# Performance work log

Measured on AMD Instinct MI355X. Metric: run time of the kernel, lower is better.

## Reference

```python
import jax, jax.numpy as jnp
import numpy as np

DIMS = 1024
HEAD = 16
CTX = 2048
BATCH = 2


def setup_inputs() -> dict:
    key = jax.random.key(0)
    ks = jax.random.split(key, 8)
    s = 0.02
    x = jax.random.normal(ks[0], (BATCH, CTX, DIMS), dtype=jnp.float32)
    Wq = jax.random.normal(ks[1], (DIMS, DIMS), dtype=jnp.float32) * s
    bq = jax.random.normal(ks[2], (DIMS,), dtype=jnp.float32) * s
    Wk = jax.random.normal(ks[3], (DIMS, DIMS), dtype=jnp.float32) * s  # k Linear has bias=False
    Wv = jax.random.normal(ks[4], (DIMS, DIMS), dtype=jnp.float32) * s
    bv = jax.random.normal(ks[5], (DIMS,), dtype=jnp.float32) * s
    Wout = jax.random.normal(ks[6], (DIMS, DIMS), dtype=jnp.float32) * s
    bout = jax.random.normal(ks[7], (DIMS,), dtype=jnp.float32) * s
    factor = jnp.asarray(0.0005, dtype=jnp.float32)
    return {"x": x, "Wq": Wq, "bq": bq, "Wk": Wk, "Wv": Wv, "bv": bv,
            "Wout": Wout, "bout": bout, "factor": factor}


def reference(x, Wq, bq, Wk, Wv, bv, Wout, bout, factor):
    b, ctx, dims = x.shape
    head = HEAD
    hd = dims // head
    scale = hd ** (-0.25)  # note: torch uses (dims // head) ** -0.25

    q = x @ Wq.T + bq
    k = x @ Wk.T
    v = x @ Wv.T + bv

    # (b, head, ctx, hd)
    q = q.reshape(b, ctx, head, hd).transpose(0, 2, 1, 3)
    k = k.reshape(b, ctx, head, hd).transpose(0, 2, 1, 3)
    v = v.reshape(b, ctx, head, hd).transpose(0, 2, 1, 3)

    # per-key scaling: keys whose first feature is exactly 0 get clamped softplus(Factor)
    zero_factor = jnp.clip(jax.nn.softplus(factor), 0.0, 0.001)
    scaled_zero = jnp.where(k[:, :, :, 0] == 0, zero_factor, jnp.ones((), x.dtype))  # (b,h,ctx)

    qk = jnp.einsum('bhqd,bhkd->bhqk', q * scale, k * scale)
    qk = qk * scaled_zero[:, :, None, :]  # broadcast over query dim
    qk = qk.astype(jnp.float32)

    w = jax.nn.softmax(qk, axis=-1)  # temperature = 1.0
    wv = jnp.einsum('bhqk,bhkd->bqhd', w, v).reshape(b, ctx, dims)

    # faithful to source: out projection applied twice (inside _forward, then in forward)
    out1 = wv @ Wout.T + bout
    out = out1 @ Wout.T + bout
    return out, qk
```

## Files before the change

kernel.cpp:

```cpp
#include <hip/hip_runtime.h>

typedef unsigned short u16;
typedef __bf16 bf16x8 __attribute__((ext_vector_type(8)));
typedef float f32x4 __attribute__((ext_vector_type(4)));
typedef unsigned int u32x4 __attribute__((ext_vector_type(4)));

__device__ __forceinline__ u16 f2b(float f) {
    union { float f; unsigned u; } c; c.f = f;
    unsigned r = (c.u + 0x7fffu + ((c.u >> 16) & 1u)) >> 16;
    return (u16)r;
}

__device__ __forceinline__ bf16x8 ldlds(const u16* p) {
    return __builtin_bit_cast(bf16x8, *(const u32x4*)p);
}

__device__ __forceinline__ void stage8(const float* s, u16* d) {
    float4 a = *(const float4*)s;
    float4 b = *(const float4*)(s + 4);
    ushort4 lo; lo.x = f2b(a.x); lo.y = f2b(a.y); lo.z = f2b(a.z); lo.w = f2b(a.w);
    ushort4 hi; hi.x = f2b(b.x); hi.y = f2b(b.y); hi.z = f2b(b.z); hi.w = f2b(b.w);
    *(ushort4*)d = lo;
    *(ushort4*)(d + 4) = hi;
}
__device__ __forceinline__ void stage8(const u16* s, u16* d) {
    *(u32x4*)d = *(const u32x4*)s;
}

__device__ __forceinline__ void cstore(float v, u16* p) { *p = f2b(v); }
__device__ __forceinline__ void cstore(float v, float* p) { *p = v; }

__global__ __launch_bounds__(256) void cvt_bf16(
    const float* __restrict__ in, u16* __restrict__ out, int n8)
{
    int i = blockIdx.x * 256 + threadIdx.x;
    if (i >= n8) return;
    const float* s = in + (size_t)i * 8;
    float4 a = *(const float4*)s;
    float4 b = *(const float4*)(s + 4);
    ushort4 lo; lo.x = f2b(a.x); lo.y = f2b(a.y); lo.z = f2b(a.z); lo.w = f2b(a.w);
    ushort4 hi; hi.x = f2b(b.x); hi.y = f2b(b.y); hi.z = f2b(b.z); hi.w = f2b(b.w);
    u16* d = out + (size_t)i * 8;
    *(ushort4*)d = lo;
    *(ushort4*)(d + 4) = hi;
}

template <typename TA, typename TB, typename TC>
__global__ __launch_bounds__(256) void gemm_bt(
    const TA* __restrict__ A, const TB* __restrict__ Bm,
    const float* __restrict__ bias, TC* __restrict__ C,
    int M, int N, int K)
{
    __shared__ u16 As[128 * 40];
    __shared__ u16 Bs[64 * 40];
    const int tid = threadIdx.x;
    const int wave = tid >> 6, lane = tid & 63, lq = lane >> 4, l15 = lane & 15;
    const int wr = wave >> 1, wc = wave & 1;

    const int hwid = blockIdx.y * gridDim.x + blockIdx.x;
    const int nwg = gridDim.x * gridDim.y;
    const int swz = (hwid & 7) * (nwg >> 3) + (hwid >> 3);
    const int tx = swz / gridDim.y;
    const int ty = swz % gridDim.y;
    const size_t m0 = (size_t)tx * 128, n0 = (size_t)ty * 64;

    f32x4 acc[4][2];
#pragma unroll
    for (int i = 0; i < 4; ++i)
#pragma unroll
        for (int j = 0; j < 2; ++j) acc[i][j] = (f32x4){0.f, 0.f, 0.f, 0.f};

    for (int k0 = 0; k0 < K; k0 += 32) {
#pragma unroll
        for (int g = 0; g < 2; ++g) {
            int c = tid + g * 256;
            int row = c >> 2, col8 = (c & 3) * 8;
            stage8(&A[(m0 + row) * (size_t)K + k0 + col8], &As[row * 40 + col8]);
        }
        {
            int row = tid >> 2, col8 = (tid & 3) * 8;
            stage8(&Bm[(n0 + row) * (size_t)K + k0 + col8], &Bs[row * 40 + col8]);
        }
        __syncthreads();
        bf16x8 af[4], bfr[2];
#pragma unroll
        for (int i = 0; i < 4; ++i)
            af[i] = ldlds(&As[(wr * 64 + i * 16 + l15) * 40 + lq * 8]);
#pragma unroll
        for (int j = 0; j < 2; ++j)
            bfr[j] = ldlds(&Bs[(wc * 32 + j * 16 + l15) * 40 + lq * 8]);
#pragma unroll
        for (int i = 0; i < 4; ++i)
#pragma unroll
            for (int j = 0; j < 2; ++j)
                acc[i][j] = __builtin_amdgcn_mfma_f32_16x16x32_bf16(
                    af[i], bfr[j], acc[i][j], 0, 0, 0);
        __syncthreads();
    }
#pragma unroll
    for (int j = 0; j < 2; ++j) {
        int n = (int)n0 + wc * 32 + j * 16 + l15;
        float bv = bias ? bias[n] : 0.0f;
#pragma unroll
        for (int i = 0; i < 4; ++i) {
            int mb = (int)m0 + wr * 64 + i * 16 + lq * 4;
#pragma unroll
            for (int r = 0; r < 4; ++r)
                cstore(acc[i][j][r] + bv, &C[(size_t)(mb + r) * N + n]);
        }
    }
}

__global__ __launch_bounds__(256) void attn_kernel(
    const u16* __restrict__ qb, const u16* __restrict__ kb,
    const u16* __restrict__ vb, const float* __restrict__ factor,
    float* __restrict__ qk_out, u16* __restrict__ wv_out)
{
    const int SCTX = 2048, SD = 1024;
    __shared__ u16 qs[64 * 72];
    __shared__ u16 ks[64 * 72];
    __shared__ u16 vts[64 * 72];
    __shared__ u16 ps[64 * 72];
    __shared__ float zf[64];

    const int tid = threadIdx.x;
    const int wave = tid >> 6, lane = tid & 63, lq = lane >> 4, l15 = lane & 15;

    const int hwid = (blockIdx.z * gridDim.y + blockIdx.y) * gridDim.x + blockIdx.x;
    const int swz = (hwid & 7) * 128 + (hwid >> 3);
    const int q0 = (swz & 31) * 64, h = (swz >> 5) & 15, b = swz >> 9;

    float zfac = log1pf(expf(factor[0]));
    zfac = fminf(fmaxf(zfac, 0.0f), 0.001f);

    const int srow = tid >> 3, scol = (tid & 7) * 8;
    const int vkrow = tid & 63, vd0 = ((tid >> 6) & 7) * 8;

    const size_t qbase = ((size_t)(b * SCTX + q0)) * SD + h * 64;
#pragma unroll
    for (int g = 0; g < 2; ++g) {
        int row = srow + g * 32;
        *(u32x4*)&qs[row * 72 + scol] =
            *(const u32x4*)&qb[qbase + (size_t)row * SD + scol];
    }
    {
        const size_t kbase = ((size_t)(b * SCTX)) * SD + h * 64;
#pragma unroll
        for (int g = 0; g < 2; ++g) {
            int row = srow + g * 32;
            *(u32x4*)&ks[row * 72 + scol] =
                *(const u32x4*)&kb[kbase + (size_t)row * SD + scol];
        }
#pragma unroll
        for (int g = 0; g < 2; ++g) {
            int d8 = vd0 + g * 32;
            u32x4 vv = *(const u32x4*)&vb[kbase + (size_t)vkrow * SD + d8];
#pragma unroll
            for (int j = 0; j < 8; ++j) {
                unsigned uu = vv[j >> 1];
                u16 e = (j & 1) ? (u16)(uu >> 16) : (u16)(uu & 0xffffu);
                vts[(d8 + j) * 72 + vkrow] = e;
            }
        }
        if (tid < 64) {
            u16 k0v = kb[kbase + (size_t)tid * SD];
            zf[tid] = ((k0v & 0x7fffu) == 0) ? zfac : 1.0f;
        }
    }
    __syncthreads();
    bf16x8 aq0 = ldlds(&qs[(wave * 16 + l15) * 72 + lq * 8]);
    bf16x8 aq1 = ldlds(&qs[(wave * 16 + l15) * 72 + lq * 8 + 32]);

    f32x4 oacc[4];
#pragma unroll
    for (int t = 0; t < 4; ++t) oacc[t] = (f32x4){0.f, 0.f, 0.f, 0.f};
    float mrun[4], lrun[4];
#pragma unroll
    for (int r = 0; r < 4; ++r) { mrun[r] = -3.0e38f; lrun[r] = 0.0f; }

    const size_t qkrow0 = ((size_t)((b * 16 + h) * SCTX + q0)) * SCTX;

    for (int kt = 0; kt < 32; ++kt) {
        u32x4 pk0, pk1, pv0, pv1; u16 pz = 0;
        const bool pre = (kt + 1 < 32);
        if (pre) {
            const size_t kb1 = ((size_t)(b * SCTX + (kt + 1) * 64)) * SD + h * 64;
            pk0 = *(const u32x4*)&kb[kb1 + (size_t)srow * SD + scol];
            pk1 = *(const u32x4*)&kb[kb1 + (size_t)(srow + 32) * SD + scol];
            pv0 = *(const u32x4*)&vb[kb1 + (size_t)vkrow * SD + vd0];
            pv1 = *(const u32x4*)&vb[kb1 + (size_t)vkrow * SD + vd0 + 32];
            if (tid < 64) pz = kb[kb1 + (size_t)tid * SD];
        }

        f32x4 sacc[4];
#pragma unroll
        for (int t = 0; t < 4; ++t) sacc[t] = (f32x4){0.f, 0.f, 0.f, 0.f};
#pragma unroll
        for (int t = 0; t < 4; ++t) {
            bf16x8 bk0 = ldlds(&ks[(t * 16 + l15) * 72 + lq * 8]);
            bf16x8 bk1 = ldlds(&ks[(t * 16 + l15) * 72 + lq * 8 + 32]);
            sacc[t] = __builtin_amdgcn_mfma_f32_16x16x32_bf16(aq0, bk0, sacc[t], 0, 0, 0);
            sacc[t] = __builtin_amdgcn_mfma_f32_16x16x32_bf16(aq1, bk1, sacc[t], 0, 0, 0);
        }
        float zfc[4];
#pragma unroll
        for (int t = 0; t < 4; ++t) zfc[t] = zf[t * 16 + l15] * 0.125f;
#pragma unroll
        for (int t = 0; t < 4; ++t)
#pragma unroll
            for (int r = 0; r < 4; ++r) sacc[t][r] *= zfc[t];
#pragma unroll
        for (int t = 0; t < 4; ++t)
#pragma unroll
            for (int r = 0; r < 4; ++r) {
                int row = wave * 16 + lq * 4 + r;
                __builtin_nontemporal_store(sacc[t][r],
                    &qk_out[qkrow0 + (size_t)row * SCTX + kt * 64 + t * 16 + l15]);
            }
#pragma unroll
        for (int r = 0; r < 4; ++r) {
            float mx = fmaxf(fmaxf(sacc[0][r], sacc[1][r]),
                             fmaxf(sacc[2][r], sacc[3][r]));
            mx = fmaxf(mx, __shfl_xor(mx, 1, 64));
            mx = fmaxf(mx, __shfl_xor(mx, 2, 64));
            mx = fmaxf(mx, __shfl_xor(mx, 4, 64));
            mx = fmaxf(mx, __shfl_xor(mx, 8, 64));
            float mnew = fmaxf(mrun[r], mx);
            float alpha = __expf(mrun[r] - mnew);
            float p0 = __expf(sacc[0][r] - mnew);
            float p1 = __expf(sacc[1][r] - mnew);
            float p2 = __expf(sacc[2][r] - mnew);
            float p3 = __expf(sacc[3][r] - mnew);
            float rs = p0 + p1 + p2 + p3;
            rs += __shfl_xor(rs, 1, 64);
            rs += __shfl_xor(rs, 2, 64);
            rs += __shfl_xor(rs, 4, 64);
            rs += __shfl_xor(rs, 8, 64);
            lrun[r] = lrun[r] * alpha + rs;
            mrun[r] = mnew;
            int prow = (wave * 16 + lq * 4 + r) * 72;
            ps[prow + 0 + l15] = f2b(p0);
            ps[prow + 16 + l15] = f2b(p1);
            ps[prow + 32 + l15] = f2b(p2);
            ps[prow + 48 + l15] = f2b(p3);
#pragma unroll
            for (int td = 0; td < 4; ++td) oacc[td][r] *= alpha;
        }
        bf16x8 ap0 = ldlds(&ps[(wave * 16 + l15) * 72 + lq * 8]);
        bf16x8 ap1 = ldlds(&ps[(wave * 16 + l15) * 72 + lq * 8 + 32]);
#pragma unroll
        for (int td = 0; td < 4; ++td) {
            bf16x8 bv0 = ldlds(&vts[(td * 16 + l15) * 72 + lq * 8]);
            bf16x8 bv1 = ldlds(&vts[(td * 16 + l15) * 72 + lq * 8 + 32]);
            oacc[td] = __builtin_amdgcn_mfma_f32_16x16x32_bf16(ap0, bv0, oacc[td], 0, 0, 0);
            oacc[td] = __builtin_amdgcn_mfma_f32_16x16x32_bf16(ap1, bv1, oacc[td], 0, 0, 0);
        }

        __syncthreads();
        if (pre) {
            *(u32x4*)&ks[srow * 72 + scol] = pk0;
            *(u32x4*)&ks[(srow + 32) * 72 + scol] = pk1;
#pragma unroll
            for (int j = 0; j < 8; ++j) {
                unsigned uu = pv0[j >> 1];
                u16 e = (j & 1) ? (u16)(uu >> 16) : (u16)(uu & 0xffffu);
                vts[(vd0 + j) * 72 + vkrow] = e;
            }
#pragma unroll
            for (int j = 0; j < 8; ++j) {
                unsigned uu = pv1[j >> 1];
                u16 e = (j & 1) ? (u16)(uu >> 16) : (u16)(uu & 0xffffu);
                vts[(vd0 + 32 + j) * 72 + vkrow] = e;
            }
            if (tid < 64) zf[tid] = ((pz & 0x7fffu) == 0) ? zfac : 1.0f;
            __syncthreads();
        }
    }
    float linv[4];
#pragma unroll
    for (int r = 0; r < 4; ++r) linv[r] = 1.0f / lrun[r];
#pragma unroll
    for (int td = 0; td < 4; ++td)
#pragma unroll
        for (int r = 0; r < 4; ++r) {
            int row = wave * 16 + lq * 4 + r;
            wv_out[qbase + (size_t)row * SD + td * 16 + l15] =
                f2b(oacc[td][r] * linv[r]);
        }
}

extern "C" void kernel_launch(void* const* d_in, const int* in_sizes, int n_in,
                              void* d_out, int out_size, void* d_ws, size_t ws_size,
                              hipStream_t stream)
{
    (void)in_sizes; (void)n_in; (void)out_size;
    const float* x      = (const float*)d_in[0];
    const float* Wq     = (const float*)d_in[1];
    const float* bq     = (const float*)d_in[2];
    const float* Wk     = (const float*)d_in[3];
    const float* Wv     = (const float*)d_in[4];
    const float* bvv    = (const float*)d_in[5];
    const float* Wout   = (const float*)d_in[6];
    const float* bout   = (const float*)d_in[7];
    const float* factor = (const float*)d_in[8];

    u16* ws   = (u16*)d_ws;
    u16* qbuf = ws;
    u16* kbuf = ws + 4194304;
    u16* vbuf = ws + 8388608;
    u16* woutb = ws + 12582912;
    const bool have_woutb = ws_size >= (size_t)27262976;

    float* outp = (float*)d_out;
    float* qkp  = outp + 4194304;
    u16* wvo  = (u16*)d_out;
    u16* out1 = qbuf;

    u16* xb  = (u16*)qkp;
    u16* wqb = xb  + 4194304;
    u16* wkb = wqb + 1048576;
    u16* wvb = wkb + 1048576;

    cvt_bf16<<<2048, 256, 0, stream>>>(x,  xb,  524288);
    cvt_bf16<<<512,  256, 0, stream>>>(Wq, wqb, 131072);
    cvt_bf16<<<512,  256, 0, stream>>>(Wk, wkb, 131072);
    cvt_bf16<<<512,  256, 0, stream>>>(Wv, wvb, 131072);
    if (have_woutb)
        cvt_bf16<<<512, 256, 0, stream>>>(Wout, woutb, 131072);

    dim3 gg(32, 16);

    gemm_bt<u16, u16, u16><<<gg, 256, 0, stream>>>(xb, wqb, bq,      qbuf, 4096, 1024, 1024);
    gemm_bt<u16, u16, u16><<<gg, 256, 0, stream>>>(xb, wkb, nullptr, kbuf, 4096, 1024, 1024);
    gemm_bt<u16, u16, u16><<<gg, 256, 0, stream>>>(xb, wvb, bvv,     vbuf, 4096, 1024, 1024);

    attn_kernel<<<dim3(32, 16, 2), 256, 0, stream>>>(qbuf, kbuf, vbuf, factor, qkp, wvo);

    if (have_woutb) {
        gemm_bt<u16, u16, u16><<<gg, 256, 0, stream>>>(wvo,  woutb, bout, out1, 4096, 1024, 1024);
        gemm_bt<u16, u16, float><<<gg, 256, 0, stream>>>(out1, woutb, bout, outp, 4096, 1024, 1024);
    } else {
        gemm_bt<u16, float, u16><<<gg, 256, 0, stream>>>(wvo,  Wout, bout, out1, 4096, 1024, 1024);
        gemm_bt<u16, float, float><<<gg, 256, 0, stream>>>(out1, Wout, bout, outp, 4096, 1024, 1024);
    }
}
```

Before: 767.4 us.

## Fold double output projection into one GEMM and use direct global-to-LDS loads

Precomputes G = Wout·Wout and a combined bias b2 = Wout·bout + bout, so the two back-to-back output projections collapse into one 4096x1024 GEMM after a small 1024^3 GEMM. It also fuses the five fp32->bf16 conversion launches into one kernel and adds a GEMM variant that loads tiles with global_load_lds into an XOR-swizzled unpadded LDS layout. The merged path needs a larger workspace and changes the rounding, since the product of weights is rounded to bf16 once instead of rounding the intermediate activations.

```diff
diff --git a/kernel.cpp b/kernel.cpp
--- a/kernel.cpp
+++ b/kernel.cpp
@@ -13,6 +13,12 @@
 
 __device__ __forceinline__ bf16x8 ldlds(const u16* p) {
     return __builtin_bit_cast(bf16x8, *(const u32x4*)p);
+}
+
+__device__ __forceinline__ void glds16(const u16* g, u16* l) {
+    __builtin_amdgcn_global_load_lds(
+        (const __attribute__((address_space(1))) unsigned*)g,
+        (__attribute__((address_space(3))) unsigned*)l, 16, 0, 0);
 }
 
 __device__ __forceinline__ void stage8(const float* s, u16* d) {
@@ -30,19 +36,126 @@
 __device__ __forceinline__ void cstore(float v, u16* p) { *p = f2b(v); }
 __device__ __forceinline__ void cstore(float v, float* p) { *p = v; }
 
-__global__ __launch_bounds__(256) void cvt_bf16(
-    const float* __restrict__ in, u16* __restrict__ out, int n8)
+__global__ __launch_bounds__(256) void cvt_all(
+    const float* __restrict__ x,  const float* __restrict__ wq,
+    const float* __restrict__ wk, const float* __restrict__ wv,
+    const float* __restrict__ wo,
+    u16* __restrict__ xb, u16* __restrict__ wqb, u16* __restrict__ wkb,
+    u16* __restrict__ wvb, u16* __restrict__ wob)
 {
     int i = blockIdx.x * 256 + threadIdx.x;
-    if (i >= n8) return;
-    const float* s = in + (size_t)i * 8;
-    float4 a = *(const float4*)s;
-    float4 b = *(const float4*)(s + 4);
+    const float* s; u16* d; int off;
+    if (i < 524288)      { s = x;  d = xb;  off = i; }
+    else if (i < 655360) { s = wq; d = wqb; off = i - 524288; }
+    else if (i < 786432) { s = wk; d = wkb; off = i - 655360; }
+    else if (i < 917504) { s = wv; d = wvb; off = i - 786432; }
+    else                 { s = wo; d = wob; off = i - 917504; }
+    const float* sp = s + (size_t)off * 8;
+    float4 a = *(const float4*)sp;
+    float4 b = *(const float4*)(sp + 4);
     ushort4 lo; lo.x = f2b(a.x); lo.y = f2b(a.y); lo.z = f2b(a.z); lo.w = f2b(a.w);
     ushort4 hi; hi.x = f2b(b.x); hi.y = f2b(b.y); hi.z = f2b(b.z); hi.w = f2b(b.w);
-    u16* d = out + (size_t)i * 8;
-    *(ushort4*)d = lo;
-    *(ushort4*)(d + 4) = hi;
+    u16* dp = d + (size_t)off * 8;
+    *(ushort4*)dp = lo;
+    *(ushort4*)(dp + 4) = hi;
+}
+
+__global__ __launch_bounds__(256) void cvt_bf16_t(
+    const float* __restrict__ in, u16* __restrict__ out)
+{
+    __shared__ float t[32][33];
+    const int i0 = blockIdx.x * 32, j0 = blockIdx.y * 32;
+    const int r = threadIdx.x >> 3, c4 = (threadIdx.x & 7) * 4;
+    float4 v = *(const float4*)&in[(size_t)(i0 + r) * 1024 + j0 + c4];
+    t[r][c4] = v.x; t[r][c4 + 1] = v.y; t[r][c4 + 2] = v.z; t[r][c4 + 3] = v.w;
+    __syncthreads();
+    ushort4 o;
+    o.x = f2b(t[c4][r]);     o.y = f2b(t[c4 + 1][r]);
+    o.z = f2b(t[c4 + 2][r]); o.w = f2b(t[c4 + 3][r]);
+    *(ushort4*)&out[(size_t)(j0 + r) * 1024 + i0 + c4] = o;
+}
+
+__global__ __launch_bounds__(64) void bias2_kernel(
+    const float* __restrict__ W, const float* __restrict__ b,
+    float* __restrict__ b2)
+{
+    const int n = blockIdx.x, l = threadIdx.x;
+    float s = 0.0f;
+    for (int j = l; j < 1024; j += 64) s += W[(size_t)n * 1024 + j] * b[j];
+#pragma unroll
+    for (int o = 1; o < 64; o <<= 1) s += __shfl_xor(s, o, 64);
+    if (l == 0) b2[n] = s + b[n];
+}
+
+template <typename TC>
+__global__ __launch_bounds__(256) void gemm_bt_gl(
+    const u16* __restrict__ A, const u16* __restrict__ Bm,
+    const float* __restrict__ bias, TC* __restrict__ C,
+    int M, int N, int K)
+{
+    __shared__ __align__(16) u16 As[128 * 32];
+    __shared__ __align__(16) u16 Bs[64 * 32];
+    const int tid = threadIdx.x;
+    const int wave = tid >> 6, lane = tid & 63, lq = lane >> 4, l15 = lane & 15;
+    const int wr = wave >> 1, wc = wave & 1;
+
+    const int hwid = blockIdx.y * gridDim.x + blockIdx.x;
+    const int nwg = gridDim.x * gridDim.y;
+    const int swz = (hwid & 7) * (nwg >> 3) + (hwid >> 3);
+    const int tx = swz / gridDim.y, ty = swz % gridDim.y;
+    const size_t m0 = (size_t)tx * 128, n0 = (size_t)ty * 64;
+
+    const int csrc = ((lane & 3) ^ ((lane >> 3) & 3)) * 8;
+    const int arow0 = wave * 32 + (lane >> 2);
+    const int brow = wave * 16 + (lane >> 2);
+    const u16* pa0 = A + (m0 + arow0) * (size_t)K + csrc;
+    const u16* pa1 = A + (m0 + arow0 + 16) * (size_t)K + csrc;
+    const u16* pb = Bm + (n0 + brow) * (size_t)K + csrc;
+    u16* la0 = &As[wave * 1024];
+    u16* la1 = &As[wave * 1024 + 512];
+    u16* lb = &Bs[wave * 512];
+
+    f32x4 acc[4][2];
+#pragma unroll
+    for (int i = 0; i < 4; ++i)
+#pragma unroll
+        for (int j = 0; j < 2; ++j) acc[i][j] = (f32x4){0.f, 0.f, 0.f, 0.f};
+
+    const int sx = (lq ^ ((l15 >> 1) & 3)) * 8;
+
+    for (int k0 = 0; k0 < K; k0 += 32) {
+        glds16(pa0, la0);
+        glds16(pa1, la1);
+        glds16(pb, lb);
+        pa0 += 32; pa1 += 32; pb += 32;
+        __syncthreads();
+        bf16x8 af[4], bfr[2];
+#pragma unroll
+        for (int i = 0; i < 4; ++i)
+            af[i] = ldlds(&As[(wr * 64 + i * 16 + l15) * 32 + sx]);
+#pragma unroll
+        for (int j = 0; j < 2; ++j)
+            bfr[j] = ldlds(&Bs[(wc * 32 + j * 16 + l15) * 32 + sx]);
+#pragma unroll
+        for (int i = 0; i < 4; ++i)
+#pragma unroll
+            for (int j = 0; j < 2; ++j)
+                acc[i][j] = __builtin_amdgcn_mfma_f32_16x16x32_bf16(
+                    af[i], bfr[j], acc[i][j], 0, 0, 0);
+        __syncthreads();
+    }
+#pragma unroll
+    for (int j = 0; j < 2; ++j) {
+        int n = (int)n0 + wc * 32 + j * 16 + l15;
+        float bv = bias ? bias[n] : 0.0f;
+#pragma unroll
+        for (int i = 0; i < 4; ++i) {
+            int mb = (int)m0 + wr * 64 + i * 16 + lq * 4;
+#pragma unroll
+            for (int r = 0; r < 4; ++r)
+                cstore(acc[i][j][r] + bv, &C[(size_t)(mb + r) * N + n]);
+        }
+    }
 }
 
 template <typename TA, typename TB, typename TC>
@@ -51,8 +164,8 @@
     const float* __restrict__ bias, TC* __restrict__ C,
     int M, int N, int K)
 {
-    __shared__ u16 As[128 * 40];
-    __shared__ u16 Bs[64 * 40];
+    __shared__ __align__(16) u16 As[128 * 40];
+    __shared__ __align__(16) u16 Bs[64 * 40];
     const int tid = threadIdx.x;
     const int wave = tid >> 6, lane = tid & 63, lq = lane >> 4, l15 = lane & 15;
     const int wr = wave >> 1, wc = wave & 1;
@@ -60,8 +173,7 @@
     const int hwid = blockIdx.y * gridDim.x + blockIdx.x;
     const int nwg = gridDim.x * gridDim.y;
     const int swz = (hwid & 7) * (nwg >> 3) + (hwid >> 3);
-    const int tx = swz / gridDim.y;
-    const int ty = swz % gridDim.y;
+    const int tx = swz / gridDim.y, ty = swz % gridDim.y;
     const size_t m0 = (size_t)tx * 128, n0 = (size_t)ty * 64;
 
     f32x4 acc[4][2];
@@ -117,10 +229,10 @@
     float* __restrict__ qk_out, u16* __restrict__ wv_out)
 {
     const int SCTX = 2048, SD = 1024;
-    __shared__ u16 qs[64 * 72];
-    __shared__ u16 ks[64 * 72];
-    __shared__ u16 vts[64 * 72];
-    __shared__ u16 ps[64 * 72];
+    __shared__ __align__(16) u16 qs[64 * 72];
+    __shared__ __align__(16) u16 ks[64 * 72];
+    __shared__ __align__(16) u16 vts[64 * 72];
+    __shared__ __align__(16) u16 ps[64 * 72];
     __shared__ float zf[64];
 
     const int tid = threadIdx.x;
@@ -309,38 +421,57 @@
     u16* kbuf = ws + 4194304;
     u16* vbuf = ws + 8388608;
     u16* woutb = ws + 12582912;
-    const bool have_woutb = ws_size >= (size_t)27262976;
+    u16* wvws  = ws + 12582912;
+    u16* Gb    = ws + 16777216;
+    float* b2f = (float*)(ws + 17825792);
+    const bool merged      = ws_size >= (size_t)35655680;
+    const bool have_woutb  = !merged && ws_size >= (size_t)27262976;
 
     float* outp = (float*)d_out;
     float* qkp  = outp + 4194304;
     u16* wvo  = (u16*)d_out;
     u16* out1 = qbuf;
 
-    u16* xb  = (u16*)qkp;
-    u16* wqb = xb  + 4194304;
-    u16* wkb = wqb + 1048576;
-    u16* wvb = wkb + 1048576;
-
-    cvt_bf16<<<2048, 256, 0, stream>>>(x,  xb,  524288);
-    cvt_bf16<<<512,  256, 0, stream>>>(Wq, wqb, 131072);
-    cvt_bf16<<<512,  256, 0, stream>>>(Wk, wkb, 131072);
-    cvt_bf16<<<512,  256, 0, stream>>>(Wv, wvb, 131072);
-    if (have_woutb)
-        cvt_bf16<<<512, 256, 0, stream>>>(Wout, woutb, 131072);
+    u16* xb   = (u16*)qkp;
+    u16* wqb  = xb + 4194304;
+    u16* wkb  = wqb + 1048576;
+    u16* wvb  = wkb + 1048576;
+    u16* wob  = wvb + 1048576;
+    u16* wotb = wob + 1048576;
+
+    u16* wo_dst = have_woutb ? woutb : wob;
+
+    cvt_all<<<4096, 256, 0, stream>>>(x, Wq, Wk, Wv, Wout,
+                                      xb, wqb, wkb, wvb, wo_dst);
 
     dim3 gg(32, 16);
 
-    gemm_bt<u16, u16, u16><<<gg, 256, 0, stream>>>(xb, wqb, bq,      qbuf, 4096, 1024, 1024);
-    gemm_bt<u16, u16, u16><<<gg, 256, 0, stream>>>(xb, wkb, nullptr, kbuf, 4096, 1024, 1024);
-    gemm_bt<u16, u16, u16><<<gg, 256, 0, stream>>>(xb, wvb, bvv,     vbuf, 4096, 1024, 1024);
-
-    attn_kernel<<<dim3(32, 16, 2), 256, 0, stream>>>(qbuf, kbuf, vbuf, factor, qkp, wvo);
-
-    if (have_woutb) {
-        gemm_bt<u16, u16, u16><<<gg, 256, 0, stream>>>(wvo,  woutb, bout, out1, 4096, 1024, 1024);
-        gemm_bt<u16, u16, float><<<gg, 256, 0, stream>>>(out1, woutb, bout, outp, 4096, 1024, 1024);
+    gemm_bt_gl<u16><<<gg, 256, 0, stream>>>(xb, wqb, bq,      qbuf, 4096, 1024, 1024);
+    gemm_bt_gl<u16><<<gg, 256, 0, stream>>>(xb, wkb, nullptr, kbuf, 4096, 1024, 1024);
+    gemm_bt_gl<u16><<<gg, 256, 0, stream>>>(xb, wvb, bvv,     vbuf, 4096, 1024, 1024);
+
+    if (merged) {
+        cvt_bf16_t<<<dim3(32, 32), 256, 0, stream>>>(Wout, wotb);
+        bias2_kernel<<<1024, 64, 0, stream>>>(Wout, bout, b2f);
+        gemm_bt_gl<u16><<<dim3(8, 16), 256, 0, stream>>>(wob, wotb, nullptr,
+                                                         Gb, 1024, 1024, 1024);
+        attn_kernel<<<dim3(32, 16, 2), 256, 0, stream>>>(qbuf, kbuf, vbuf,
+                                                         factor, qkp, wvws);
+        gemm_bt_gl<float><<<gg, 256, 0, stream>>>(wvws, Gb, b2f, outp,
+                                                  4096, 1024, 1024);
     } else {
-        gemm_bt<u16, float, u16><<<gg, 256, 0, stream>>>(wvo,  Wout, bout, out1, 4096, 1024, 1024);
-        gemm_bt<u16, float, float><<<gg, 256, 0, stream>>>(out1, Wout, bout, outp, 4096, 1024, 1024);
-    }
-}
+        attn_kernel<<<dim3(32, 16, 2), 256, 0, stream>>>(qbuf, kbuf, vbuf,
+                                                         factor, qkp, wvo);
+        if (have_woutb) {
+            gemm_bt_gl<u16><<<gg, 256, 0, stream>>>(wvo, woutb, bout, out1,
+                                                    4096, 1024, 1024);
+            gemm_bt_gl<float><<<gg, 256, 0, stream>>>(out1, woutb, bout, outp,
+                                                      4096, 1024, 1024);
+        } else {
+            gemm_bt<u16, float, u16><<<gg, 256, 0, stream>>>(
+                wvo, Wout, bout, out1, 4096, 1024, 1024);
+            gemm_bt<u16, float, float><<<gg, 256, 0, stream>>>(
+                out1, Wout, bout, outp, 4096, 1024, 1024);
+        }
+    }
+}
```

After: 751.5 us. -2.1%, faster.
